# Performance work log

Measured on AMD Instinct MI355X. Metric: run time of the kernel, lower is better.

The kernel has to match this reference:

```python
import jax, jax.numpy as jnp
from jax import lax
import numpy as np


def _dilate3x3(img):
    # Faithful to torch: zero-pad by 1 (f.pad default), then 3x3 max over the
    # padded window (strel of ones => plain max, zeros from padding included).
    imgp = jnp.pad(img, ((0, 0), (0, 0), (1, 1), (1, 1)))
    return lax.reduce_window(imgp, -jnp.inf, lax.max,
                             (1, 1, 3, 3), (1, 1, 1, 1), 'VALID')


def setup_inputs() -> dict:
    key = jax.random.key(0)
    x = jax.random.normal(key, (32, 3, 512, 512), dtype=jnp.float32)
    return {"in_tensor": x, "n_pixels": 20}


def reference(in_tensor, n_pixels):
    # smoother = linspace(1, 0, n+1); smoother_diff = -diff => 1/n per step (linear)
    smoother = jnp.linspace(1.0, 0.0, n_pixels + 1)
    sdiff = (-jnp.diff(smoother)).astype(in_tensor.dtype)  # [n_pixels]

    def step(carry, w):
        out, img = carry
        out = out + w * img
        img = _dilate3x3(img)
        return (out, img), None

    init = (jnp.zeros_like(in_tensor), in_tensor)
    (out, _), _ = lax.scan(step, init, sdiff)
    return out
```

## Files before the change

kernel.cpp:

```cpp
#include <hip/hip_runtime.h>

#define IMG_W 512
#define IMG_H 512
#define TILE 88
#define HALO 20
#define NSTEP 19
#define RH 8
#define RW 8
#define REG 128

__device__ __forceinline__ float max3f(float a, float b, float c) {
    return fmaxf(fmaxf(a, b), c);
}

__device__ __forceinline__ float dpp_shr1(float v) {
    int i = __builtin_bit_cast(int, v);
    i = __builtin_amdgcn_update_dpp(i, i, 0x111, 0xf, 0xf, false);
    return __builtin_bit_cast(float, i);
}
__device__ __forceinline__ float dpp_shl1(float v) {
    int i = __builtin_bit_cast(int, v);
    i = __builtin_amdgcn_update_dpp(i, i, 0x101, 0xf, 0xf, false);
    return __builtin_bit_cast(float, i);
}

template<bool MASKED>
__device__ __forceinline__ void hrow(const float (&Ar)[RW], const float (&colm)[RW],
                                     float (&h)[RW]) {
    float hl = dpp_shr1(Ar[RW - 1]);
    float hr = dpp_shl1(Ar[0]);
    h[0] = max3f(hl, Ar[0], Ar[1]);
    #pragma unroll
    for (int c = 1; c < RW - 1; ++c) h[c] = max3f(Ar[c - 1], Ar[c], Ar[c + 1]);
    h[RW - 1] = max3f(Ar[RW - 2], Ar[RW - 1], hr);
    if (MASKED) {
        #pragma unroll
        for (int c = 0; c < RW; ++c) h[c] *= colm[c];
    }
}

template<bool EDGE>
__device__ __forceinline__ void body(const float* __restrict__ xc, float* __restrict__ oc,
                                     int gx0, int gy0, int tx, int ty,
                                     float4 (*topH4)[2][16][16], float4 (*botH4)[2][16][16]) {
    const int rx = tx * RW;
    const int ry = ty * RH;
    const int gx = gx0 + rx;
    const int gy = gy0 + ry;

    float A[RH][RW];
    float acc[RH][RW];
    float rowm[RH], colm[RW];

    if (EDGE) {
        #pragma unroll
        for (int c = 0; c < RW; ++c) {
            int xx = gx + c;
            colm[c] = (xx >= 0 && xx < IMG_W) ? 1.f : 0.f;
        }
        #pragma unroll
        for (int r = 0; r < RH; ++r) {
            int yy = gy + r;
            rowm[r] = (yy >= 0 && yy < IMG_H) ? 1.f : 0.f;
        }
        #pragma unroll
        for (int r = 0; r < RH; ++r) {
            int yy = min(max(gy + r, 0), IMG_H - 1);
            const float* rp = xc + (size_t)yy * IMG_W;
            #pragma unroll
            for (int c = 0; c < RW; ++c) {
                int xx = min(max(gx + c, 0), IMG_W - 1);
                float v = rp[xx] * (rowm[r] * colm[c]);
                A[r][c] = v;
                acc[r][c] = v;
            }
        }
    } else {
        #pragma unroll
        for (int c = 0; c < RW; ++c) colm[c] = 1.f;
        #pragma unroll
        for (int r = 0; r < RH; ++r) rowm[r] = 1.f;
        #pragma unroll
        for (int r = 0; r < RH; ++r) {
            const float4* rp = (const float4*)(xc + (size_t)(gy + r) * IMG_W + gx);
            float4 v0 = rp[0], v1 = rp[1];
            A[r][0] = v0.x; A[r][1] = v0.y; A[r][2] = v0.z; A[r][3] = v0.w;
            A[r][4] = v1.x; A[r][5] = v1.y; A[r][6] = v1.z; A[r][7] = v1.w;
            #pragma unroll
            for (int c = 0; c < RW; ++c) acc[r][c] = A[r][c];
        }
    }

    #pragma unroll 1
    for (int s = 0; s < NSTEP; ++s) {
        const int buf = s & 1;
        float hc[RW], h7[RW];
        hrow<EDGE>(A[0], colm, hc);
        hrow<EDGE>(A[RH - 1], colm, h7);
        topH4[buf][0][ty][tx] = make_float4(hc[0], hc[1], hc[2], hc[3]);
        topH4[buf][1][ty][tx] = make_float4(hc[4], hc[5], hc[6], hc[7]);
        botH4[buf][0][ty][tx] = make_float4(h7[0], h7[1], h7[2], h7[3]);
        botH4[buf][1][ty][tx] = make_float4(h7[4], h7[5], h7[6], h7[7]);
        __syncthreads();
        const int tyu = ty > 0  ? ty - 1 : 0;
        const int tyd = ty < 15 ? ty + 1 : 15;
        float hm1[RW], hbot[RW];
        {
            float4 u0 = botH4[buf][0][tyu][tx], u1 = botH4[buf][1][tyu][tx];
            float4 d0 = topH4[buf][0][tyd][tx], d1 = topH4[buf][1][tyd][tx];
            hm1[0] = u0.x; hm1[1] = u0.y; hm1[2] = u0.z; hm1[3] = u0.w;
            hm1[4] = u1.x; hm1[5] = u1.y; hm1[6] = u1.z; hm1[7] = u1.w;
            hbot[0] = d0.x; hbot[1] = d0.y; hbot[2] = d0.z; hbot[3] = d0.w;
            hbot[4] = d1.x; hbot[5] = d1.y; hbot[6] = d1.z; hbot[7] = d1.w;
        }
        #pragma unroll
        for (int r = 0; r < RH; ++r) {
            float hn[RW];
            if (r < RH - 2) {
                hrow<EDGE>(A[r + 1], colm, hn);
            } else if (r == RH - 2) {
                #pragma unroll
                for (int c = 0; c < RW; ++c) hn[c] = h7[c];
            } else {
                #pragma unroll
                for (int c = 0; c < RW; ++c) hn[c] = hbot[c];
            }
            #pragma unroll
            for (int c = 0; c < RW; ++c) {
                float v = max3f(hm1[c], hc[c], hn[c]);
                if (EDGE) v *= rowm[r];
                A[r][c] = v;
                acc[r][c] += v;
            }
            #pragma unroll
            for (int c = 0; c < RW; ++c) { hm1[c] = hc[c]; hc[c] = hn[c]; }
        }
    }

    if (EDGE) {
        #pragma unroll
        for (int r = 0; r < RH; ++r) {
            const int rr = ry + r;
            const int yy = gy0 + rr;
            if (rr >= HALO && rr < HALO + TILE && yy < IMG_H) {
                #pragma unroll
                for (int c = 0; c < RW; ++c) {
                    const int cc = rx + c;
                    const int xx = gx0 + cc;
                    if (cc >= HALO && cc < HALO + TILE && xx < IMG_W)
                        oc[(size_t)yy * IMG_W + xx] = 0.05f * acc[r][c];
                }
            }
        }
    } else {
        #pragma unroll
        for (int r = 0; r < RH; ++r) {
            const int rr = ry + r;
            if (rr < HALO || rr >= HALO + TILE) continue;
            const int yy = gy0 + rr;
            float* rowp = oc + (size_t)yy * IMG_W + gx;
            if (tx >= 3 && tx <= 12) {
                ((float4*)rowp)[0] = make_float4(0.05f * acc[r][0], 0.05f * acc[r][1],
                                                 0.05f * acc[r][2], 0.05f * acc[r][3]);
                ((float4*)rowp)[1] = make_float4(0.05f * acc[r][4], 0.05f * acc[r][5],
                                                 0.05f * acc[r][6], 0.05f * acc[r][7]);
            } else if (tx == 2) {
                ((float4*)rowp)[1] = make_float4(0.05f * acc[r][4], 0.05f * acc[r][5],
                                                 0.05f * acc[r][6], 0.05f * acc[r][7]);
            } else if (tx == 13) {
                ((float4*)rowp)[0] = make_float4(0.05f * acc[r][0], 0.05f * acc[r][1],
                                                 0.05f * acc[r][2], 0.05f * acc[r][3]);
            }
        }
    }
}

__global__ __launch_bounds__(256, 2)
void blur_outwards_kernel(const float* __restrict__ x, float* __restrict__ out) {
    __shared__ float4 topH4[2][2][16][16];
    __shared__ float4 botH4[2][2][16][16];

    const int tid = threadIdx.x;
    const int tx = tid & 15;
    const int ty = tid >> 4;

    const int ch  = blockIdx.z;
    const int gx0 = (int)blockIdx.x * TILE - HALO;
    const int gy0 = (int)blockIdx.y * TILE - HALO;

    const float* __restrict__ xc = x + (size_t)ch * (IMG_W * IMG_H);
    float* __restrict__ oc = out + (size_t)ch * (IMG_W * IMG_H);

    const bool interior = (gx0 >= 0) && (gy0 >= 0) &&
                          (gx0 + REG <= IMG_W) && (gy0 + REG <= IMG_H);
    if (interior) body<false>(xc, oc, gx0, gy0, tx, ty, topH4, botH4);
    else          body<true >(xc, oc, gx0, gy0, tx, ty, topH4, botH4);
}

extern "C" void kernel_launch(void* const* d_in, const int* in_sizes, int n_in,
                              void* d_out, int out_size, void* d_ws, size_t ws_size,
                              hipStream_t stream) {
    const float* x = (const float*)d_in[0];
    float* out = (float*)d_out;
    dim3 grid((IMG_W + TILE - 1) / TILE,
              (IMG_H + TILE - 1) / TILE,
              96);
    blur_outwards_kernel<<<grid, 256, 0, stream>>>(x, out);
}
```

Baseline: 309.1 us.

## Replace edge zero-masking with distance-based floor; single-buffer exchange; raise occupancy

Edge tiles no longer multiply every horizontal and vertical max by 0/1 column and row masks. Instead, each pixel takes a max with 0 once its distance to the image border is within the current dilation step, which reproduces the repeated zero padding with fewer operations. The shared halo exchange drops from double to single buffering, which adds a barrier per step but halves shared memory. The launch bound rises to 4 blocks per CU, which may force register spills given the 64-element A and acc arrays held per thread.

```diff
diff --git a/kernel.cpp b/kernel.cpp
--- a/kernel.cpp
+++ b/kernel.cpp
@@ -8,6 +8,7 @@
 #define RH 8
 #define RW 8
 #define REG 128
+#define NINF (-1.0e30f)
 
 __device__ __forceinline__ float max3f(float a, float b, float c) {
     return fmaxf(fmaxf(a, b), c);
@@ -24,25 +25,20 @@
     return __builtin_bit_cast(float, i);
 }
 
-template<bool MASKED>
-__device__ __forceinline__ void hrow(const float (&Ar)[RW], const float (&colm)[RW],
-                                     float (&h)[RW]) {
+__device__ __forceinline__ void hrow(const float (&Ar)[RW], float (&h)[RW]) {
     float hl = dpp_shr1(Ar[RW - 1]);
     float hr = dpp_shl1(Ar[0]);
     h[0] = max3f(hl, Ar[0], Ar[1]);
     #pragma unroll
     for (int c = 1; c < RW - 1; ++c) h[c] = max3f(Ar[c - 1], Ar[c], Ar[c + 1]);
     h[RW - 1] = max3f(Ar[RW - 2], Ar[RW - 1], hr);
-    if (MASKED) {
-        #pragma unroll
-        for (int c = 0; c < RW; ++c) h[c] *= colm[c];
-    }
-}
+}
+
+typedef float4 ExBuf[2][2][16][16];
 
 template<bool EDGE>
 __device__ __forceinline__ void body(const float* __restrict__ xc, float* __restrict__ oc,
-                                     int gx0, int gy0, int tx, int ty,
-                                     float4 (*topH4)[2][16][16], float4 (*botH4)[2][16][16]) {
+                                     int gx0, int gy0, int tx, int ty, ExBuf& ex) {
     const int rx = tx * RW;
     const int ry = ty * RH;
     const int gx = gx0 + rx;
@@ -50,36 +46,36 @@
 
     float A[RH][RW];
     float acc[RH][RW];
-    float rowm[RH], colm[RW];
+    float rdm[RH], cdm[RW];
 
     if (EDGE) {
         #pragma unroll
         for (int c = 0; c < RW; ++c) {
             int xx = gx + c;
-            colm[c] = (xx >= 0 && xx < IMG_W) ? 1.f : 0.f;
+            cdm[c] = (float)min(xx + 1, IMG_W - xx);
         }
         #pragma unroll
         for (int r = 0; r < RH; ++r) {
             int yy = gy + r;
-            rowm[r] = (yy >= 0 && yy < IMG_H) ? 1.f : 0.f;
-        }
-        #pragma unroll
-        for (int r = 0; r < RH; ++r) {
-            int yy = min(max(gy + r, 0), IMG_H - 1);
-            const float* rp = xc + (size_t)yy * IMG_W;
+            rdm[r] = (float)min(yy + 1, IMG_H - yy);
+        }
+        #pragma unroll
+        for (int r = 0; r < RH; ++r) {
+            int yy = gy + r;
+            float rm = (yy >= 0 && yy < IMG_H) ? 1.f : 0.f;
+            int yyc = min(max(yy, 0), IMG_H - 1);
+            const float* rp = xc + (size_t)yyc * IMG_W;
             #pragma unroll
             for (int c = 0; c < RW; ++c) {
-                int xx = min(max(gx + c, 0), IMG_W - 1);
-                float v = rp[xx] * (rowm[r] * colm[c]);
+                int xx = gx + c;
+                float cm = (xx >= 0 && xx < IMG_W) ? 1.f : 0.f;
+                int xxc = min(max(xx, 0), IMG_W - 1);
+                float v = rp[xxc] * (rm * cm);
                 A[r][c] = v;
                 acc[r][c] = v;
             }
         }
     } else {
-        #pragma unroll
-        for (int c = 0; c < RW; ++c) colm[c] = 1.f;
-        #pragma unroll
-        for (int r = 0; r < RH; ++r) rowm[r] = 1.f;
         #pragma unroll
         for (int r = 0; r < RH; ++r) {
             const float4* rp = (const float4*)(xc + (size_t)(gy + r) * IMG_W + gx);
@@ -93,31 +89,37 @@
 
     #pragma unroll 1
     for (int s = 0; s < NSTEP; ++s) {
-        const int buf = s & 1;
         float hc[RW], h7[RW];
-        hrow<EDGE>(A[0], colm, hc);
-        hrow<EDGE>(A[RH - 1], colm, h7);
-        topH4[buf][0][ty][tx] = make_float4(hc[0], hc[1], hc[2], hc[3]);
-        topH4[buf][1][ty][tx] = make_float4(hc[4], hc[5], hc[6], hc[7]);
-        botH4[buf][0][ty][tx] = make_float4(h7[0], h7[1], h7[2], h7[3]);
-        botH4[buf][1][ty][tx] = make_float4(h7[4], h7[5], h7[6], h7[7]);
+        hrow(A[0], hc);
+        hrow(A[RH - 1], h7);
+        if (s) __syncthreads();
+        ex[0][0][ty][tx] = make_float4(hc[0], hc[1], hc[2], hc[3]);
+        ex[0][1][ty][tx] = make_float4(hc[4], hc[5], hc[6], hc[7]);
+        ex[1][0][ty][tx] = make_float4(h7[0], h7[1], h7[2], h7[3]);
+        ex[1][1][ty][tx] = make_float4(h7[4], h7[5], h7[6], h7[7]);
         __syncthreads();
         const int tyu = ty > 0  ? ty - 1 : 0;
         const int tyd = ty < 15 ? ty + 1 : 15;
         float hm1[RW], hbot[RW];
         {
-            float4 u0 = botH4[buf][0][tyu][tx], u1 = botH4[buf][1][tyu][tx];
-            float4 d0 = topH4[buf][0][tyd][tx], d1 = topH4[buf][1][tyd][tx];
+            float4 u0 = ex[1][0][tyu][tx], u1 = ex[1][1][tyu][tx];
+            float4 d0 = ex[0][0][tyd][tx], d1 = ex[0][1][tyd][tx];
             hm1[0] = u0.x; hm1[1] = u0.y; hm1[2] = u0.z; hm1[3] = u0.w;
             hm1[4] = u1.x; hm1[5] = u1.y; hm1[6] = u1.z; hm1[7] = u1.w;
             hbot[0] = d0.x; hbot[1] = d0.y; hbot[2] = d0.z; hbot[3] = d0.w;
             hbot[4] = d1.x; hbot[5] = d1.y; hbot[6] = d1.z; hbot[7] = d1.w;
         }
+        float Lc[RW];
+        const float sf1 = (float)(s + 1);
+        if (EDGE) {
+            #pragma unroll
+            for (int c = 0; c < RW; ++c) Lc[c] = (sf1 >= cdm[c]) ? 0.f : NINF;
+        }
         #pragma unroll
         for (int r = 0; r < RH; ++r) {
             float hn[RW];
             if (r < RH - 2) {
-                hrow<EDGE>(A[r + 1], colm, hn);
+                hrow(A[r + 1], hn);
             } else if (r == RH - 2) {
                 #pragma unroll
                 for (int c = 0; c < RW; ++c) hn[c] = h7[c];
@@ -125,10 +127,12 @@
                 #pragma unroll
                 for (int c = 0; c < RW; ++c) hn[c] = hbot[c];
             }
+            float Lr;
+            if (EDGE) Lr = (sf1 >= rdm[r]) ? 0.f : NINF;
             #pragma unroll
             for (int c = 0; c < RW; ++c) {
                 float v = max3f(hm1[c], hc[c], hn[c]);
-                if (EDGE) v *= rowm[r];
+                if (EDGE) v = max3f(v, Lr, Lc[c]);
                 A[r][c] = v;
                 acc[r][c] += v;
             }
@@ -175,10 +179,9 @@
     }
 }
 
-__global__ __launch_bounds__(256, 2)
+__global__ __launch_bounds__(256, 4)
 void blur_outwards_kernel(const float* __restrict__ x, float* __restrict__ out) {
-    __shared__ float4 topH4[2][2][16][16];
-    __shared__ float4 botH4[2][2][16][16];
+    __shared__ ExBuf ex;
 
     const int tid = threadIdx.x;
     const int tx = tid & 15;
@@ -193,8 +196,8 @@
 
     const bool interior = (gx0 >= 0) && (gy0 >= 0) &&
                           (gx0 + REG <= IMG_W) && (gy0 + REG <= IMG_H);
-    if (interior) body<false>(xc, oc, gx0, gy0, tx, ty, topH4, botH4);
-    else          body<true >(xc, oc, gx0, gy0, tx, ty, topH4, botH4);
+    if (interior) body<false>(xc, oc, gx0, gy0, tx, ty, ex);
+    else          body<true >(xc, oc, gx0, gy0, tx, ty, ex);
 }
 
 extern "C" void kernel_launch(void* const* d_in, const int* in_sizes, int n_in,
```

After: 1.201 ms. +288.5%, slower.
